# Optimization experiments

Hardware: AMD Instinct MI355X
Metric: run time of the kernel (lower is better)

Reference implementation:

```python
import jax, jax.numpy as jnp
import numpy as np

WS = 8          # window size (8x8)
HEADS = 8
DIM_HEAD = 28
SCALE = DIM_HEAD ** -0.5


def _window_partition(t, ws=WS):
    # [b, H, W, c] -> [b, n_windows, ws*ws, c]
    b, H, W, c = t.shape
    t = t.reshape(b, H // ws, ws, W // ws, ws, c)
    t = t.transpose(0, 1, 3, 2, 4, 5)
    return t.reshape(b, (H // ws) * (W // ws), ws * ws, c)


def _window_reverse(t, H, W, ws=WS):
    # [b, n_windows, ws*ws, c] -> [b, H, W, c]
    b = t.shape[0]
    c = t.shape[-1]
    t = t.reshape(b, H // ws, W // ws, ws, ws, c)
    t = t.transpose(0, 1, 3, 2, 4, 5)
    return t.reshape(b, H, W, c)


def _heads_split(t, nh):
    # [b, n, mm, (nh*d)] -> [b, n, nh, mm, d]
    b, n, mm, cd = t.shape
    return t.reshape(b, n, mm, nh, cd // nh).transpose(0, 1, 3, 2, 4)


def setup_inputs() -> dict:
    key = jax.random.key(0)
    ks = jax.random.split(key, 6)
    b, H, W, c = 128, 32, 32, 224
    inner = DIM_HEAD * HEADS  # 224
    return {
        "x": jax.random.normal(ks[0], (b, H, W, c), jnp.float32),
        "Wq": jax.random.normal(ks[1], (c, inner), jnp.float32) * (c ** -0.5),
        "Wkv": jax.random.normal(ks[2], (c, 2 * inner), jnp.float32) * (c ** -0.5),
        "Wout": jax.random.normal(ks[3], (inner, c), jnp.float32) * (inner ** -0.5),
        "bout": jnp.zeros((c,), jnp.float32),
        "pos_emb1": jax.random.normal(ks[4], (1, 1, HEADS // 2, WS * WS, WS * WS), jnp.float32),
        "pos_emb2": jax.random.normal(ks[5], (1, 1, HEADS // 2, 16, 16), jnp.float32),
    }


def reference(x, Wq, Wkv, Wout, bout, pos_emb1, pos_emb2):
    b, H, W, c = x.shape
    nh = HEADS // 2  # heads per branch

    q = x @ Wq                       # [b,H,W,224]
    kv = x @ Wkv
    k, v = jnp.split(kv, 2, axis=-1)

    half = c // 2
    q1, q2 = q[..., :half], q[..., half:]
    k1, k2 = k[..., :half], k[..., half:]
    v1, v2 = v[..., :half], v[..., half:]

    # ----- local branch: attention within each 8x8 window -----
    q1 = _heads_split(_window_partition(q1), nh) * SCALE  # [b,n,nh,64,d]
    k1 = _heads_split(_window_partition(k1), nh)
    v1 = _heads_split(_window_partition(v1), nh)
    sim1 = jnp.einsum('bnhid,bnhjd->bnhij', q1, k1) + pos_emb1
    attn1 = jax.nn.softmax(sim1, axis=-1)
    out1 = jnp.einsum('bnhij,bnhjd->bnhid', attn1, v1)    # [b,n,nh,64,d]
    bN = out1.shape[1]
    out1 = out1.transpose(0, 1, 3, 2, 4).reshape(b, bN, WS * WS, half)

    # ----- global branch: attention across windows (same in-window position) -----
    def part_global(t):
        t = _window_partition(t)                 # [b,n,mm,half]
        t = t.transpose(0, 2, 1, 3)              # [b,mm,n,half]
        return _heads_split(t, nh)               # [b,mm,nh,n,d]
    q2 = part_global(q2) * SCALE
    k2 = part_global(k2)
    v2 = part_global(v2)
    sim2 = jnp.einsum('bnhid,bnhjd->bnhij', q2, k2) + pos_emb2
    attn2 = jax.nn.softmax(sim2, axis=-1)
    out2 = jnp.einsum('bnhij,bnhjd->bnhid', attn2, v2)    # [b,mm,nh,n,d]
    out2 = out2.transpose(0, 1, 3, 2, 4).reshape(b, WS * WS, bN, half)
    out2 = out2.transpose(0, 2, 1, 3)                     # [b,n,mm,half]

    out = jnp.concatenate([out1, out2], axis=-1)          # [b,n,mm,c]
    out = out @ Wout + bout
    return _window_reverse(out, H, W)
```

## Files before the change

kernel.cpp:

```cpp
#include <hip/hip_runtime.h>
#include <stdint.h>

typedef short s8v __attribute__((ext_vector_type(8)));
typedef float f4v __attribute__((ext_vector_type(4)));
typedef unsigned short u16;

#define MFMA16(a, b, c) __builtin_amdgcn_mfma_f32_16x16x32_bf16(a, b, c, 0, 0, 0)
#define SCALE 0.1889822365046136f

__device__ __forceinline__ u16 f2bf(float f) {
  union { float f; uint32_t u; } v;
  v.f = f;
  uint32_t u = v.u;
  u += 0x7fffu + ((u >> 16) & 1u);
  return (u16)(u >> 16);
}

__device__ __forceinline__ void gld_lds16(const void* g, void* l) {
  __builtin_amdgcn_global_load_lds(
      (const __attribute__((address_space(1))) void*)g,
      (__attribute__((address_space(3))) void*)l, 16, 0, 0);
}

__global__ void prep_kernel(const float4* __restrict__ x4,
                            const float* __restrict__ Wq,
                            const float* __restrict__ Wkv,
                            const float* __restrict__ Wout,
                            u16* __restrict__ xb,
                            u16* __restrict__ wqkvt,
                            u16* __restrict__ woutt) {
  const int gsz = gridDim.x * blockDim.x;
  const int gt = blockIdx.x * blockDim.x + threadIdx.x;
  for (int i = gt; i < 7340032; i += gsz) {
    float4 v = x4[i];
    ushort4 o;
    o.x = f2bf(v.x); o.y = f2bf(v.y); o.z = f2bf(v.z); o.w = f2bf(v.w);
    ((ushort4*)xb)[i] = o;
  }
  for (int i = gt; i < 768 * 224; i += gsz) {
    const int n = i / 224, k = i - n * 224;
    float v = 0.f;
    if (n < 224) v = Wq[k * 224 + n];
    else if (n < 672) v = Wkv[k * 448 + (n - 224)];
    wqkvt[i] = f2bf(v);
  }
  for (int i = gt; i < 256 * 224; i += gsz) {
    const int n = i / 224, k = i - n * 224;
    const float v = (n < 224) ? Wout[k * 224 + n] : 0.f;
    woutt[i] = f2bf(v);
  }
}

template <int OUT_F32, int NTILES>
__global__ __launch_bounds__(256) void gemm_af(const u16* __restrict__ Ap,
                                               const u16* __restrict__ Bt,
                                               void* __restrict__ Cp,
                                               const float* __restrict__ bias,
                                               int Nvalid, int ldc) {
  extern __shared__ u16 smem[];
  u16* As  = smem;
  u16* Bs0 = smem + 28672;
  u16* Bs1 = smem + 32768;
  const int tid = threadIdx.x;
  const int wave = tid >> 6, lane = tid & 63;
  const int c16 = lane & 15, g = lane >> 4;
  const int m0 = blockIdx.x * 128;
  const int wm = wave & 1, wn = wave >> 1;

  const int fbw = wave * 1024 + lane * 16;
  const int brow0 = fbw >> 6, bcol0 = (fbw & 63) >> 1;

#define STAGE_B(ntile, ktile, bufp)                                            \
  do {                                                                         \
    char* bb = (char*)((bufp) ? Bs1 : Bs0) + wave * 1024;                      \
    const u16* src =                                                           \
        Bt + (size_t)((ntile) * 128 + brow0) * 224 + (ktile) * 32 + bcol0;     \
    gld_lds16(src, bb);                                                        \
    gld_lds16(src + (size_t)64 * 224, bb + 4096);                              \
  } while (0)

  STAGE_B(0, 0, 0);
  if (NTILES * 7 > 1) STAGE_B(0, 1, 1);

  for (int rnd = 0; rnd < 14; ++rnd) {
    const int fb = rnd * 4096 + fbw;
    const int row = fb / 448;
    const int off = fb - row * 448;
    gld_lds16(Ap + (size_t)(m0 + row) * 224 + (off >> 1),
              (char*)As + rnd * 4096 + wave * 1024);
  }
  __syncthreads();

  for (int nt = 0; nt < NTILES; ++nt) {
    f4v acc[4][4] = {};
    for (int kt = 0; kt < 7; ++kt) {
      const int t = nt * 7 + kt;
      const u16* Bs = (t & 1) ? Bs1 : Bs0;
      s8v af[4], bf[4];
      for (int tt = 0; tt < 4; ++tt)
        af[tt] = *(const s8v*)&As[(wm * 64 + tt * 16 + c16) * 224 + kt * 32 + g * 8];
      for (int tt = 0; tt < 4; ++tt)
        bf[tt] = *(const s8v*)&Bs[(wn * 64 + tt * 16 + c16) * 32 + g * 8];
      for (int i = 0; i < 4; ++i)
        for (int j = 0; j < 4; ++j)
          acc[i][j] = MFMA16(af[i], bf[j], acc[i][j]);
      __syncthreads();
      const int ns = t + 2;
      if (ns < NTILES * 7) {
        const int nnt = ns / 7;
        STAGE_B(nnt, ns - nnt * 7, t & 1);
      }
    }
    const int n0 = nt * 128;
    for (int i = 0; i < 4; ++i) {
      const int rowb = m0 + wm * 64 + i * 16 + g * 4;
      for (int j = 0; j < 4; ++j) {
        const int col = n0 + wn * 64 + j * 16 + c16;
        if (col < Nvalid) {
          if (OUT_F32) {
            const float bz = bias[col];
            for (int r = 0; r < 4; ++r)
              ((float*)Cp)[(size_t)(rowb + r) * ldc + col] = acc[i][j][r] + bz;
          } else {
            for (int r = 0; r < 4; ++r)
              ((u16*)Cp)[(size_t)(rowb + r) * ldc + col] = f2bf(acc[i][j][r]);
          }
        }
      }
    }
  }
#undef STAGE_B
}

__global__ __launch_bounds__(256, 2) void attn_fused(
    const u16* __restrict__ xb, const u16* __restrict__ Wt,
    const float* __restrict__ pos1, const float* __restrict__ pos2,
    u16* __restrict__ attn) {
  extern __shared__ u16 sm[];
  u16* As  = sm;
  u16* Bs0 = sm + 14336;
  u16* Bs1 = sm + 25088;
  const int blk0 = blockIdx.x;
  const int local = (blk0 < 2048) ? 1 : 0;
  const int blk = local ? blk0 : blk0 - 2048;
  const int tid = threadIdx.x;
  const int wave = tid >> 6, lane = tid & 63;
  const int c16 = lane & 15, g = lane >> 4;
  const int b = blk >> 4, sub = blk & 15;

  int base_s = 0, ig = 0;
  if (local) {
    base_s = (b * 32 + (sub >> 2) * 8) * 32 + (sub & 3) * 8;
  } else {
    ig = sub;
  }

#pragma unroll
  for (int m = 0; m < 7; ++m) {
    const int chunk = m * 256 + tid;
    const int row = chunk / 28;
    const int c = chunk - row * 28;
    int s;
    if (local) {
      s = base_s + (row >> 3) * 32 + (row & 7);
    } else {
      const int w2 = row >> 4, j = row & 15;
      const int ii = ig * 4 + w2;
      const int y = ii >> 3, x = ii & 7;
      s = (b * 32 + (j >> 2) * 8 + y) * 32 + (j & 3) * 8 + x;
    }
    gld_lds16(xb + (size_t)s * 224 + c * 8, (char*)As + chunk * 16);
  }

  const int qoff = local ? 0 : 112;
#define STAGE_W(ktile, buf)                                                   \
  do {                                                                        \
    for (int mm = 0; mm < 6; ++mm) {                                          \
      const int ch = mm * 256 + tid;                                          \
      if (ch < 1344) {                                                        \
        const int brow = ch >> 2, bc = (ch & 3) * 8;                          \
        const int n = qoff + brow + ((brow >= 112) ? 112 : 0) +               \
                      ((brow >= 224) ? 112 : 0);                              \
        gld_lds16(Wt + (size_t)n * 224 + (ktile) * 32 + bc,                   \
                  (char*)(buf) + ch * 16);                                    \
      }                                                                       \
    }                                                                         \
  } while (0)

  STAGE_W(0, Bs0);
  STAGE_W(1, Bs1);
  __syncthreads();

  f4v acc[6][4] = {};
  for (int kt = 0; kt < 7; ++kt) {
    const u16* Bs = (kt & 1) ? Bs1 : Bs0;
    s8v af[4];
#pragma unroll
    for (int st = 0; st < 4; ++st)
      af[st] = *(const s8v*)&As[(st * 16 + c16) * 224 + kt * 32 + g * 8];
#pragma unroll
    for (int j = 0; j < 6; ++j) {
      const int tile = j * 4 + wave;
      if (tile < 21) {
        const s8v bf = *(const s8v*)&Bs[(tile * 16 + c16) * 32 + g * 8];
#pragma unroll
        for (int st = 0; st < 4; ++st)
          acc[j][st] = MFMA16(af[st], bf, acc[j][st]);
      }
    }
    __syncthreads();
    if (kt + 2 < 7) STAGE_W(kt + 2, (kt & 1) ? Bs1 : Bs0);
  }

  u16* qs  = sm;
  u16* ks  = sm + 8192;
  u16* vtL = sm + 18432;
  u16* vtG = sm + 16384;
  u16* pm  = sm;
  u16* p2  = sm + 24608;

#pragma unroll
  for (int j = 0; j < 6; ++j) {
    const int tile = j * 4 + wave;
    if (tile < 21) {
      const int seg = (tile >= 14) ? 2 : ((tile >= 7) ? 1 : 0);
      const int nn = tile * 16 + c16 - seg * 112;
      const int h = ((nn >= 28) ? 1 : 0) + ((nn >= 56) ? 1 : 0) + ((nn >= 84) ? 1 : 0);
      const int d = nn - h * 28;
#pragma unroll
      for (int st = 0; st < 4; ++st) {
        if (seg == 2) {
          ushort4 o;
          o.x = f2bf(acc[j][st][0]); o.y = f2bf(acc[j][st][1]);
          o.z = f2bf(acc[j][st][2]); o.w = f2bf(acc[j][st][3]);
          if (local)
            *(ushort4*)&vtL[(h * 32 + d) * 72 + st * 16 + g * 4] = o;
          else
            *(ushort4*)&vtG[st * 2056 + (h * 32 + d) * 16 + g * 4] = o;
        } else {
          u16* dst = seg ? ks : qs;
#pragma unroll
          for (int r = 0; r < 4; ++r) {
            const u16 v = f2bf(acc[j][st][r]);
            if (local)
              dst[(h * 64 + st * 16 + g * 4 + r) * 32 + d] = v;
            else
              dst[((st * 4 + h) * 16 + g * 4 + r) * 32 + d] = v;
          }
        }
      }
    }
  }
  {
    const ushort4 z = {0, 0, 0, 0};
    *(ushort4*)(qs + tid * 32 + 28) = z;
    *(ushort4*)(ks + tid * 32 + 28) = z;
    if (!local) {
      const int w2 = tid >> 6, hq = (tid >> 4) & 3;
      const int dd = 28 + ((tid >> 2) & 3), j4 = tid & 3;
      *(ushort4*)(vtG + w2 * 2056 + (hq * 32 + dd) * 16 + j4 * 4) = z;
    }
  }
  __syncthreads();

  const f4v fz = {0.f, 0.f, 0.f, 0.f};
  if (local) {
    const int h = wave;
    s8v af2[4], bf2[4];
    for (int t = 0; t < 4; ++t)
      af2[t] = *(const s8v*)&qs[(h * 64 + t * 16 + c16) * 32 + g * 8];
    for (int t = 0; t < 4; ++t)
      bf2[t] = *(const s8v*)&ks[(h * 64 + t * 16 + c16) * 32 + g * 8];
    f4v sc[4][4];
    for (int i = 0; i < 4; ++i)
      for (int j = 0; j < 4; ++j)
        sc[i][j] = MFMA16(af2[i], bf2[j], fz);
    float lrow[4][4];
    const float* ph = pos1 + h * 4096;
    for (int i = 0; i < 4; ++i) {
      for (int r = 0; r < 4; ++r) {
        const int irow = i * 16 + g * 4 + r;
        float mx = -1e30f;
        for (int j = 0; j < 4; ++j) {
          const float v = sc[i][j][r] * SCALE + ph[irow * 64 + j * 16 + c16];
          sc[i][j][r] = v;
          mx = fmaxf(mx, v);
        }
        for (int dd = 1; dd < 16; dd <<= 1) mx = fmaxf(mx, __shfl_xor(mx, dd, 64));
        float sum = 0.f;
        for (int j = 0; j < 4; ++j) {
          const float e = __expf(sc[i][j][r] - mx);
          sc[i][j][r] = e;
          sum += e;
        }
        for (int dd = 1; dd < 16; dd <<= 1) sum += __shfl_xor(sum, dd, 64);
        lrow[i][r] = sum;
      }
    }
    __syncthreads();
    for (int i = 0; i < 4; ++i)
      for (int r = 0; r < 4; ++r) {
        const int irow = i * 16 + g * 4 + r;
        for (int j = 0; j < 4; ++j)
          pm[(h * 64 + irow) * 72 + j * 16 + c16] = f2bf(sc[i][j][r]);
      }
    f4v o[4][2] = {};
    for (int kk = 0; kk < 2; ++kk) {
      s8v ap[4], bv[2];
      for (int t = 0; t < 4; ++t)
        ap[t] = *(const s8v*)&pm[(h * 64 + t * 16 + c16) * 72 + kk * 32 + g * 8];
      for (int t = 0; t < 2; ++t)
        bv[t] = *(const s8v*)&vtL[(h * 32 + t * 16 + c16) * 72 + kk * 32 + g * 8];
      for (int i = 0; i < 4; ++i)
        for (int j = 0; j < 2; ++j)
          o[i][j] = MFMA16(ap[i], bv[j], o[i][j]);
    }
    for (int i = 0; i < 4; ++i)
      for (int r = 0; r < 4; ++r) {
        const int irow = i * 16 + g * 4 + r;
        const int s = base_s + (irow >> 3) * 32 + (irow & 7);
        const float inv = 1.f / lrow[i][r];
        for (int j = 0; j < 2; ++j) {
          const int d = j * 16 + c16;
          if (d < 28)
            attn[(size_t)s * 224 + h * 28 + d] = f2bf(o[i][j][r] * inv);
        }
      }
  } else {
    const int w = wave;
    const int i = ig * 4 + w;
    const int y = i >> 3, x = i & 7;
    const int w4 = w * 4;
    for (int h = 0; h < 4; ++h) {
      const s8v aq = *(const s8v*)&qs[((w4 + h) * 16 + c16) * 32 + g * 8];
      const s8v bk = *(const s8v*)&ks[((w4 + h) * 16 + c16) * 32 + g * 8];
      const f4v s = MFMA16(aq, bk, fz);
      const float* ph = pos2 + h * 256;
      float l[4];
      for (int r = 0; r < 4; ++r) {
        const float v = s[r] * SCALE + ph[(g * 4 + r) * 16 + c16];
        float mx = v;
        for (int dd = 1; dd < 16; dd <<= 1) mx = fmaxf(mx, __shfl_xor(mx, dd, 64));
        const float e = __expf(v - mx);
        float sum = e;
        for (int dd = 1; dd < 16; dd <<= 1) sum += __shfl_xor(sum, dd, 64);
        l[r] = sum;
        p2[(w * 16 + g * 4 + r) * 32 + c16] = f2bf(e);
        p2[(w * 16 + g * 4 + r) * 32 + c16 + 16] = 0;
      }
      const s8v ap = *(const s8v*)&p2[(w * 16 + c16) * 32 + g * 8];
      f4v o[2];
      for (int nt = 0; nt < 2; ++nt) {
        s8v bv = {0, 0, 0, 0, 0, 0, 0, 0};
        if (g < 2)
          bv = *(const s8v*)&vtG[w * 2056 + (h * 32 + nt * 16 + c16) * 16 + g * 8];
        o[nt] = MFMA16(ap, bv, fz);
      }
      for (int nt = 0; nt < 2; ++nt)
        for (int r = 0; r < 4; ++r) {
          const int d = nt * 16 + c16;
          if (d < 28) {
            const int wi = g * 4 + r;
            const int sw = (b * 32 + (wi >> 2) * 8 + y) * 32 + (wi & 3) * 8 + x;
            attn[(size_t)sw * 224 + 112 + h * 28 + d] = f2bf(o[nt][r] / l[r]);
          }
        }
    }
  }
#undef STAGE_W
}

extern "C" void kernel_launch(void* const* d_in, const int* in_sizes, int n_in,
                              void* d_out, int out_size, void* d_ws, size_t ws_size,
                              hipStream_t stream) {
  const float* x    = (const float*)d_in[0];
  const float* Wq   = (const float*)d_in[1];
  const float* Wkv  = (const float*)d_in[2];
  const float* Wout = (const float*)d_in[3];
  const float* bout = (const float*)d_in[4];
  const float* pos1 = (const float*)d_in[5];
  const float* pos2 = (const float*)d_in[6];
  char* ws = (char*)d_ws;
  u16* xb    = (u16*)ws;
  u16* attn  = (u16*)(ws + 58720256);
  u16* wqkvt = (u16*)(ws + 117440512);
  u16* woutt = (u16*)(ws + 117784576);

  prep_kernel<<<dim3(1024), 256, 0, stream>>>(
      (const float4*)x, Wq, Wkv, Wout, xb, wqkvt, woutt);

  attn_fused<<<dim3(4096), 256, 71680, stream>>>(xb, wqkvt, pos1, pos2, attn);

  gemm_af<1, 2><<<dim3(1024), 256, 73728, stream>>>(attn, woutt, d_out, bout, 224, 224);
}
```

Baseline: 368.8 us.

## Double-buffer x tiles per k-step to cut LDS and raise occupancy

Instead of staging the whole 64x224 activation block into LDS up front, the fused attention kernel now streams 64x32 k-tiles of x through two small buffers alongside the weight tiles. The V-transpose layout is compacted (stride 28 per head instead of 32) so the attention phase fits into less shared memory. Dynamic LDS drops from 71680 to 53568 bytes and launch bounds go from 2 to 3 blocks per CU, aiming at higher occupancy to hide latency. The risk is extra register pressure under the tighter launch bound and overlapping V rows between heads in the compacted layout, which may cause correctness issues.

```diff
diff --git a/kernel.cpp b/kernel.cpp
--- a/kernel.cpp
+++ b/kernel.cpp
@@ -132,14 +132,15 @@
 #undef STAGE_B
 }
 
-__global__ __launch_bounds__(256, 2) void attn_fused(
+__global__ __launch_bounds__(256, 3) void attn_fused(
     const u16* __restrict__ xb, const u16* __restrict__ Wt,
     const float* __restrict__ pos1, const float* __restrict__ pos2,
     u16* __restrict__ attn) {
   extern __shared__ u16 sm[];
-  u16* As  = sm;
-  u16* Bs0 = sm + 14336;
-  u16* Bs1 = sm + 25088;
+  u16* As0 = sm;
+  u16* As1 = sm + 2048;
+  u16* Bs0 = sm + 4096;
+  u16* Bs1 = sm + 14848;
   const int blk0 = blockIdx.x;
   const int local = (blk0 < 2048) ? 1 : 0;
   const int blk = local ? blk0 : blk0 - 2048;
@@ -155,22 +156,23 @@
     ig = sub;
   }
 
-#pragma unroll
-  for (int m = 0; m < 7; ++m) {
-    const int chunk = m * 256 + tid;
-    const int row = chunk / 28;
-    const int c = chunk - row * 28;
-    int s;
+  int s_a;
+  {
+    const int arow = tid >> 2;
     if (local) {
-      s = base_s + (row >> 3) * 32 + (row & 7);
+      s_a = base_s + (arow >> 3) * 32 + (arow & 7);
     } else {
-      const int w2 = row >> 4, j = row & 15;
+      const int w2 = arow >> 4, j = arow & 15;
       const int ii = ig * 4 + w2;
       const int y = ii >> 3, x = ii & 7;
-      s = (b * 32 + (j >> 2) * 8 + y) * 32 + (j & 3) * 8 + x;
-    }
-    gld_lds16(xb + (size_t)s * 224 + c * 8, (char*)As + chunk * 16);
-  }
+      s_a = (b * 32 + (j >> 2) * 8 + y) * 32 + (j & 3) * 8 + x;
+    }
+  }
+  const int a_off = (tid & 3) * 8;
+
+#define STAGE_A(ktile, buf)                                                   \
+  gld_lds16(xb + (size_t)s_a * 224 + (ktile) * 32 + a_off,                    \
+            (char*)(buf) + tid * 16)
 
   const int qoff = local ? 0 : 112;
 #define STAGE_W(ktile, buf)                                                   \
@@ -187,17 +189,20 @@
     }                                                                         \
   } while (0)
 
+  STAGE_A(0, As0);
   STAGE_W(0, Bs0);
+  STAGE_A(1, As1);
   STAGE_W(1, Bs1);
   __syncthreads();
 
   f4v acc[6][4] = {};
   for (int kt = 0; kt < 7; ++kt) {
     const u16* Bs = (kt & 1) ? Bs1 : Bs0;
+    const u16* Asb = (kt & 1) ? As1 : As0;
     s8v af[4];
 #pragma unroll
     for (int st = 0; st < 4; ++st)
-      af[st] = *(const s8v*)&As[(st * 16 + c16) * 224 + kt * 32 + g * 8];
+      af[st] = *(const s8v*)&Asb[(st * 16 + c16) * 32 + g * 8];
 #pragma unroll
     for (int j = 0; j < 6; ++j) {
       const int tile = j * 4 + wave;
@@ -209,14 +214,17 @@
       }
     }
     __syncthreads();
-    if (kt + 2 < 7) STAGE_W(kt + 2, (kt & 1) ? Bs1 : Bs0);
+    if (kt + 2 < 7) {
+      STAGE_A(kt + 2, (kt & 1) ? As1 : As0);
+      STAGE_W(kt + 2, (kt & 1) ? Bs1 : Bs0);
+    }
   }
 
   u16* qs  = sm;
   u16* ks  = sm + 8192;
+  u16* pm  = sm;
   u16* vtL = sm + 18432;
   u16* vtG = sm + 16384;
-  u16* pm  = sm;
   u16* p2  = sm + 24608;
 
 #pragma unroll
@@ -234,7 +242,7 @@
           o.x = f2bf(acc[j][st][0]); o.y = f2bf(acc[j][st][1]);
           o.z = f2bf(acc[j][st][2]); o.w = f2bf(acc[j][st][3]);
           if (local)
-            *(ushort4*)&vtL[(h * 32 + d) * 72 + st * 16 + g * 4] = o;
+            *(ushort4*)&vtL[(h * 28 + d) * 72 + st * 16 + g * 4] = o;
           else
             *(ushort4*)&vtG[st * 2056 + (h * 32 + d) * 16 + g * 4] = o;
         } else {
@@ -310,7 +318,7 @@
       for (int t = 0; t < 4; ++t)
         ap[t] = *(const s8v*)&pm[(h * 64 + t * 16 + c16) * 72 + kk * 32 + g * 8];
       for (int t = 0; t < 2; ++t)
-        bv[t] = *(const s8v*)&vtL[(h * 32 + t * 16 + c16) * 72 + kk * 32 + g * 8];
+        bv[t] = *(const s8v*)&vtL[(h * 28 + t * 16 + c16) * 72 + kk * 32 + g * 8];
       for (int i = 0; i < 4; ++i)
         for (int j = 0; j < 2; ++j)
           o[i][j] = MFMA16(ap[i], bv[j], o[i][j]);
@@ -368,6 +376,7 @@
     }
   }
 #undef STAGE_W
+#undef STAGE_A
 }
 
 extern "C" void kernel_launch(void* const* d_in, const int* in_sizes, int n_in,
@@ -389,7 +398,7 @@
   prep_kernel<<<dim3(1024), 256, 0, stream>>>(
       (const float4*)x, Wq, Wkv, Wout, xb, wqkvt, woutt);
 
-  attn_fused<<<dim3(4096), 256, 71680, stream>>>(xb, wqkvt, pos1, pos2, attn);
+  attn_fused<<<dim3(4096), 256, 53568, stream>>>(xb, wqkvt, pos1, pos2, attn);
 
   gemm_af<1, 2><<<dim3(1024), 256, 73728, stream>>>(attn, woutt, d_out, bout, 224, 224);
 }
```

New measurement: 349.1 us. -5.3%, faster.
